# Kernel tuning notes

Measured on AMD Instinct MI355X. Metric: run time of the kernel, lower is better.

## Reference

```python
import jax, jax.numpy as jnp
import numpy as np

B, S, EMBED, DK, DV, M = 8, 1024, 1024, 512, 512, 64


def setup_inputs() -> dict:
    key = jax.random.key(0)
    ks = jax.random.split(key, 9)
    query_in = jax.random.normal(ks[0], (B, S, EMBED), dtype=jnp.float32)
    key_in = jax.random.normal(ks[1], (B, S, EMBED), dtype=jnp.float32)
    value_in = jax.random.normal(ks[2], (B, S, EMBED), dtype=jnp.float32)
    lim = 1.0 / np.sqrt(EMBED)  # nn.Linear default init range
    u = lambda k, shape: jax.random.uniform(k, shape, minval=-lim, maxval=lim, dtype=jnp.float32)
    return {
        'query_in': query_in, 'key_in': key_in, 'value_in': value_in,
        'Wq': u(ks[3], (DK, EMBED)), 'bq': u(ks[4], (DK,)),
        'Wk': u(ks[5], (DK, EMBED)), 'bk': u(ks[6], (DK,)),
        'Wv': u(ks[7], (DV, EMBED)), 'bv': u(ks[8], (DV,)),
    }


def _select_landmarks(k_proj, m):
    # Original code runs recursive RLS sampling (random, host-side) over the m
    # segment-rows of key.reshape(B, m, seg, d) and gathers m of them back,
    # then flattens to (B, S, d). We use a deterministic data-dependent
    # selection (rows ranked by squared norm) with identical gather structure.
    Bb, Ss, d = k_proj.shape
    seg = Ss // m
    kr = k_proj.reshape(Bb, m, seg, d)
    scores = jnp.sum(kr * kr, axis=(2, 3))                      # [B, m]
    idx = jnp.argsort(-scores, axis=1)                          # [B, m]
    land = jnp.take_along_axis(kr, idx[:, :, None, None], axis=1)
    return land.reshape(Bb, Ss, d)                              # [B, S, d]


def reference(query_in, key_in, value_in, Wq, bq, Wk, bk, Wv, bv):
    scaling = DK ** -0.25  # 1/sqrt(sqrt(d_k)), applied to both q and k
    q = (jnp.einsum('bse,de->bsd', query_in, Wq) + bq) * scaling
    k = (jnp.einsum('bse,de->bsd', key_in, Wk) + bk) * scaling
    v = jnp.einsum('bse,de->bsd', value_in, Wv) + bv

    kl = _select_landmarks(k, M)                                # [B, S, DK]
    # is_decoder_self_attn is hard-coded True upstream -> q_landmarks = q,
    # so kernel_2 == kernel_1.
    kernel_1 = jax.nn.softmax(jnp.einsum('bqd,bkd->bqk', q, kl), axis=-1)
    kernel_2 = kernel_1
    kernel_3 = jax.nn.softmax(jnp.einsum('bqd,bkd->bqk', q, k), axis=-1)

    k2_inv = jnp.linalg.pinv(kernel_2)                          # [B, S, S] batched SVD
    out = jnp.einsum('bqk,bkd->bqd', jnp.einsum('bqm,bmk->bqk', kernel_1, k2_inv),
                     jnp.einsum('bqk,bkd->bqd', kernel_3, v))
    # dropout is identity in eval mode
    return out
```

## Files before the change

### kernel.cpp

```cpp
#include <hip/hip_runtime.h>
#include <hip/hip_bf16.h>

#define SS   1024
#define DKK  512

typedef __hip_bfloat16 bf16;
typedef __attribute__((ext_vector_type(8))) short s16x8;
typedef __attribute__((ext_vector_type(8))) unsigned short u16x8;
typedef __attribute__((ext_vector_type(4))) float f32x4;

#define WS_W(z)  ((48ull << 20) + ((size_t)(z) << 20))
#define WS_Q     (52ull << 20)
#define WS_K     (60ull << 20)
#define WS_VT    (68ull << 20)
#define WS_LG    (0ull)

__device__ __forceinline__ void async_ld16(const void* g, void* s) {
  __builtin_amdgcn_global_load_lds(
      (const __attribute__((address_space(1))) void*)g,
      (__attribute__((address_space(3))) void*)s, 16, 0, 0);
}

__device__ __forceinline__ unsigned short f2bfu(float f) {
  return __builtin_bit_cast(unsigned short, __float2bfloat16(f));
}
__device__ __forceinline__ float bfu2f(unsigned short u) {
  unsigned int i = ((unsigned int)u) << 16;
  return __builtin_bit_cast(float, i);
}

__global__ __launch_bounds__(256)
void convert_w(const float* __restrict__ w0, const float* __restrict__ w1,
               const float* __restrict__ w2, char* __restrict__ ws)
{
  const int bx = blockIdx.x;
  const int z = bx >> 8, local = bx & 255;
  const float* src = (z == 0) ? w0 : (z == 1) ? w1 : w2;
  unsigned short* dst = (unsigned short*)(ws + WS_W(z));
  const int i = local * 2048 + threadIdx.x * 8;
  const float4* s = (const float4*)(src + i);
  float4 a = s[0], b = s[1];
  ushort4 o0, o1;
  o0.x = f2bfu(a.x); o0.y = f2bfu(a.y); o0.z = f2bfu(a.z); o0.w = f2bfu(a.w);
  o1.x = f2bfu(b.x); o1.y = f2bfu(b.y); o1.z = f2bfu(b.z); o1.w = f2bfu(b.w);
  ((ushort4*)(dst + i))[0] = o0;
  ((ushort4*)(dst + i))[1] = o1;
}

template<int BM, int K, int LDA, int LDB>
__device__ __forceinline__ void gemm_core(const bf16* __restrict__ A,
                                          const bf16* __restrict__ Bw,
                                          int bm, int bn,
                                          short* As, short* Bs, f32x4* acc)
{
  constexpr int MI = BM / 32;
  constexpr int AR = BM / 4;
  const int tid  = threadIdx.x;
  const int lane = tid & 63;
  const int wave = tid >> 6;
  const int l8   = lane >> 3;
  const int kch  = ((lane & 7) ^ l8) * 8;
  const bf16* ag = A  + (size_t)(bm * BM + wave * AR + l8) * LDA + kch;
  const bf16* bg = Bw + (size_t)(bn * 128 + wave * 32 + l8) * LDB + kch;
  short* AsW = As + wave * AR * 64;
  short* BsW = Bs + wave * 32 * 64;
  const int waveM = wave >> 1, waveN = wave & 1;
  const int l16  = lane & 15;
  const int quad = lane >> 4;
  const int xr   = l16 & 7;

  #pragma unroll
  for (int t = 0; t < MI * 4; ++t)
    #pragma unroll
    for (int r = 0; r < 4; ++r) acc[t][r] = 0.0f;

  for (int kt = 0; kt < K / 64; ++kt) {
    #pragma unroll
    for (int j = 0; j < AR / 8; ++j) async_ld16(ag + (size_t)j * 8 * LDA, AsW + j * 8 * 64);
    #pragma unroll
    for (int j = 0; j < 4; ++j)      async_ld16(bg + (size_t)j * 8 * LDB, BsW + j * 8 * 64);
    ag += 64; bg += 64;
    __syncthreads();
    #pragma unroll
    for (int ks = 0; ks < 2; ++ks) {
      s16x8 af[MI], bfv[4];
      #pragma unroll
      for (int mi = 0; mi < MI; ++mi) {
        const int row  = waveM * (BM / 2) + mi * 16 + l16;
        const int slot = (ks * 4 + quad) ^ xr;
        af[mi] = *(const s16x8*)&As[row * 64 + slot * 8];
      }
      #pragma unroll
      for (int ni = 0; ni < 4; ++ni) {
        const int row  = waveN * 64 + ni * 16 + l16;
        const int slot = (ks * 4 + quad) ^ xr;
        bfv[ni] = *(const s16x8*)&Bs[row * 64 + slot * 8];
      }
      #pragma unroll
      for (int mi = 0; mi < MI; ++mi)
        #pragma unroll
        for (int ni = 0; ni < 4; ++ni)
          acc[mi * 4 + ni] = __builtin_amdgcn_mfma_f32_16x16x32_bf16(
              af[mi], bfv[ni], acc[mi * 4 + ni], 0, 0, 0);
    }
    __syncthreads();
  }
}

template<int K, int LDA, int LDB>
__device__ __forceinline__ void gemm_core_f32a(const float* __restrict__ A,
                                               const bf16* __restrict__ Bw,
                                               int bm, int bn,
                                               short* As, short* Bs, f32x4* acc)
{
  const int tid  = threadIdx.x;
  const int lane = tid & 63;
  const int wave = tid >> 6;
  const int l8   = lane >> 3;
  const int kch  = ((lane & 7) ^ l8) * 8;
  const bf16* bg = Bw + (size_t)(bn * 256 + wave * 64 + l8) * LDB + kch;
  short* BsW = Bs + wave * 64 * 64;
  const int arow = tid >> 3;
  const int ag8  = tid & 7;
  const int slotA = (ag8 ^ (arow & 7)) * 8;
  const float* ag = A + (size_t)(bm * 64 + arow) * LDA + ag8 * 8;
  const int waveM = wave >> 1, waveN = wave & 1;
  const int l16  = lane & 15;
  const int quad = lane >> 4;
  const int xr   = l16 & 7;

  #pragma unroll
  for (int t = 0; t < 16; ++t)
    #pragma unroll
    for (int r = 0; r < 4; ++r) acc[t][r] = 0.0f;

  for (int kt = 0; kt < K / 64; ++kt) {
    #pragma unroll
    for (int j = 0; j < 8; ++j) async_ld16(bg + (size_t)j * 8 * LDB, BsW + j * 8 * 64);
    bg += 64;
    #pragma unroll
    for (int p = 0; p < 2; ++p) {
      const float4* s = (const float4*)(ag + (size_t)p * 32 * LDA);
      float4 a = s[0], b = s[1];
      u16x8 v;
      v[0] = f2bfu(a.x); v[1] = f2bfu(a.y); v[2] = f2bfu(a.z); v[3] = f2bfu(a.w);
      v[4] = f2bfu(b.x); v[5] = f2bfu(b.y); v[6] = f2bfu(b.z); v[7] = f2bfu(b.w);
      *(u16x8*)&As[(p * 32 + arow) * 64 + slotA] = v;
    }
    ag += 64;
    __syncthreads();
    #pragma unroll
    for (int ks = 0; ks < 2; ++ks) {
      s16x8 af[2], bfv[8];
      #pragma unroll
      for (int mi = 0; mi < 2; ++mi) {
        const int row  = waveM * 32 + mi * 16 + l16;
        const int slot = (ks * 4 + quad) ^ xr;
        af[mi] = *(const s16x8*)&As[row * 64 + slot * 8];
      }
      #pragma unroll
      for (int ni = 0; ni < 8; ++ni) {
        const int row  = waveN * 128 + ni * 16 + l16;
        const int slot = (ks * 4 + quad) ^ xr;
        bfv[ni] = *(const s16x8*)&Bs[row * 64 + slot * 8];
      }
      #pragma unroll
      for (int mi = 0; mi < 2; ++mi)
        #pragma unroll
        for (int ni = 0; ni < 8; ++ni)
          acc[mi * 8 + ni] = __builtin_amdgcn_mfma_f32_16x16x32_bf16(
              af[mi], bfv[ni], acc[mi * 8 + ni], 0, 0, 0);
    }
    __syncthreads();
  }
}

__global__ __launch_bounds__(256, 3)
void proj_kernel(const float* __restrict__ Xq, const float* __restrict__ Xk,
                 const float* __restrict__ Xv, const bf16* __restrict__ W0,
                 const float* __restrict__ bq, const float* __restrict__ bk,
                 const float* __restrict__ bv,
                 bf16* __restrict__ qo, bf16* __restrict__ ko,
                 bf16* __restrict__ vT, float qscale)
{
  __shared__ __align__(16) short As[64 * 64];
  __shared__ __align__(16) short Bs[256 * 64];
  const int id   = blockIdx.x;
  const int xcd  = id & 7;
  const int s    = id >> 3;
  const int bn   = s & 1;
  const int pair = (s >> 1) * 8 + xcd;
  const int bm   = pair & 127;
  const int z    = pair >> 7;
  const float* A  = (z == 0) ? Xq : (z == 1) ? Xk : Xv;
  const bf16*  Bw = W0 + ((size_t)z << 19);
  const float* bias = (z == 0) ? bq : (z == 1) ? bk : bv;
  f32x4 acc[16];
  gemm_core_f32a<1024, 1024, 1024>(A, Bw, bm, bn, As, Bs, acc);

  const int lane = threadIdx.x & 63;
  const int wave = threadIdx.x >> 6;
  const int waveM = wave >> 1, waveN = wave & 1;
  const int l16 = lane & 15, quad = lane >> 4;
  const int row0 = bm * 64 + waveM * 32;
  const int col0 = bn * 256 + waveN * 128;
  const float sc = (z == 0) ? qscale : 1.0f;
  bf16* C = (z == 0) ? qo : ko;
  #pragma unroll
  for (int ni = 0; ni < 8; ++ni) {
    const int col = col0 + ni * 16 + l16;
    const float bb = bias[col];
    #pragma unroll
    for (int mi = 0; mi < 2; ++mi)
      #pragma unroll
      for (int r = 0; r < 4; ++r) {
        const int row = row0 + mi * 16 + quad * 4 + r;
        const float v = acc[mi * 8 + ni][r] + bb;
        if (z == 2)
          vT[((size_t)(row >> 10) * DKK + col) * SS + (row & (SS - 1))] =
              __float2bfloat16(v);
        else
          C[(size_t)row * DKK + col] = __float2bfloat16(v * sc);
      }
  }
}

__global__ __launch_bounds__(256, 2)
void scores_kernel(const bf16* __restrict__ q, const bf16* __restrict__ k,
                   bf16* __restrict__ lgB)
{
  __shared__ __align__(16) short As[128 * 64];
  __shared__ __align__(16) short Bs[128 * 64];
  const int id = blockIdx.x;
  const int z  = id & 7;
  const int s  = id >> 3;
  const int bm = s & 7;
  const int bn = s >> 3;
  f32x4 acc[16];
  gemm_core<128, 512, 512, 512>(q + (size_t)z * SS * DKK, k + (size_t)z * SS * DKK,
                                bm, bn, As, Bs, acc);

  const int lane = threadIdx.x & 63;
  const int wave = threadIdx.x >> 6;
  const int waveM = wave >> 1, waveN = wave & 1;
  const int l16 = lane & 15, quad = lane >> 4;
  const int row0 = bm * 128 + waveM * 64;
  const int col0 = bn * 128 + waveN * 64;
  bf16* C = lgB + (size_t)z * SS * SS;
  #pragma unroll
  for (int ni = 0; ni < 4; ++ni) {
    const int col = col0 + ni * 16 + l16;
    #pragma unroll
    for (int mi = 0; mi < 4; ++mi)
      #pragma unroll
      for (int r = 0; r < 4; ++r) {
        const int row = row0 + mi * 16 + quad * 4 + r;
        C[(size_t)row * SS + col] = __float2bfloat16(acc[mi * 4 + ni][r]);
      }
  }
}

__global__ __launch_bounds__(256)
void softmax_p(unsigned short* __restrict__ lg)
{
  const int id = blockIdx.x;
  const int z  = id & 7;
  const int rb = id >> 3;
  const int w    = threadIdx.x >> 6;
  const int lane = threadIdx.x & 63;
  const int row  = rb * 4 + w;
  unsigned short* p = lg + ((size_t)z * SS + row) * SS + lane * 16;

  u16x8 a = *(const u16x8*)p;
  u16x8 b = *(const u16x8*)(p + 8);
  float xf[16];
  #pragma unroll
  for (int j = 0; j < 8; ++j) { xf[j] = bfu2f(a[j]); xf[8 + j] = bfu2f(b[j]); }

  float m = xf[0];
  #pragma unroll
  for (int j = 1; j < 16; ++j) m = fmaxf(m, xf[j]);
  #pragma unroll
  for (int msk = 1; msk < 64; msk <<= 1) m = fmaxf(m, __shfl_xor(m, msk));

  float e[16];
  float L = 0.f;
  #pragma unroll
  for (int j = 0; j < 16; ++j) { e[j] = __expf(xf[j] - m); L += e[j]; }
  #pragma unroll
  for (int msk = 1; msk < 64; msk <<= 1) L += __shfl_xor(L, msk);
  const float R = 1.0f / L;

  u16x8 o0, o1;
  #pragma unroll
  for (int j = 0; j < 8; ++j) {
    o0[j] = f2bfu(e[j] * R);
    o1[j] = f2bfu(e[8 + j] * R);
  }
  *(u16x8*)p = o0;
  *(u16x8*)(p + 8) = o1;
}

__global__ __launch_bounds__(256, 2)
void pv_kernel(const bf16* __restrict__ P, const bf16* __restrict__ vT,
               float* __restrict__ out)
{
  __shared__ __align__(16) short As[128 * 64];
  __shared__ __align__(16) short Bs[128 * 64];
  const int id = blockIdx.x;
  const int z  = id & 7;
  const int s  = id >> 3;
  const int bm = s & 7;
  const int bn = s >> 3;
  f32x4 acc[16];
  gemm_core<128, 1024, 1024, 1024>(P + (size_t)z * SS * SS,
                                   vT + (size_t)z * DKK * SS,
                                   bm, bn, As, Bs, acc);

  const int lane = threadIdx.x & 63;
  const int wave = threadIdx.x >> 6;
  const int waveM = wave >> 1, waveN = wave & 1;
  const int l16 = lane & 15, quad = lane >> 4;
  const int row0 = bm * 128 + waveM * 64;
  const int col0 = bn * 128 + waveN * 64;
  float* C = out + (size_t)z * SS * DKK;
  #pragma unroll
  for (int ni = 0; ni < 4; ++ni) {
    const int col = col0 + ni * 16 + l16;
    #pragma unroll
    for (int mi = 0; mi < 4; ++mi)
      #pragma unroll
      for (int r = 0; r < 4; ++r) {
        const int row = row0 + mi * 16 + quad * 4 + r;
        C[(size_t)row * DKK + col] = acc[mi * 4 + ni][r];
      }
  }
}

extern "C" void kernel_launch(void* const* d_in, const int* in_sizes, int n_in,
                              void* d_out, int out_size, void* d_ws, size_t ws_size,
                              hipStream_t stream)
{
  char* ws = (char*)d_ws;
  bf16*  W0   = (bf16*)(ws + WS_W(0));
  bf16*  q    = (bf16*)(ws + WS_Q);
  bf16*  kk   = (bf16*)(ws + WS_K);
  bf16*  vT   = (bf16*)(ws + WS_VT);
  bf16*  lgB  = (bf16*)(ws + WS_LG);

  const float qscale = 0.044194173824159216f;

  dim3 blk(256, 1, 1);
  hipLaunchKernelGGL(convert_w, dim3(768), blk, 0, stream,
                     (const float*)d_in[3], (const float*)d_in[5],
                     (const float*)d_in[7], ws);
  hipLaunchKernelGGL(proj_kernel, dim3(768, 1, 1), blk, 0, stream,
                     (const float*)d_in[0], (const float*)d_in[1],
                     (const float*)d_in[2], W0,
                     (const float*)d_in[4], (const float*)d_in[6],
                     (const float*)d_in[8], q, kk, vT, qscale);
  hipLaunchKernelGGL(scores_kernel, dim3(512, 1, 1), blk, 0, stream,
                     q, kk, lgB);
  hipLaunchKernelGGL(softmax_p, dim3(2048, 1, 1), blk, 0, stream,
                     (unsigned short*)lgB);
  hipLaunchKernelGGL(pv_kernel, dim3(256, 1, 1), blk, 0, stream,
                     lgB, vT, (float*)d_out);
}
```

Measured before the change: 217.9 us.

## Prefetch fp32 A tiles into registers and halve M tile for attention GEMMs

```diff
diff --git a/kernel.cpp b/kernel.cpp
--- a/kernel.cpp
+++ b/kernel.cpp
@@ -134,21 +134,36 @@
     #pragma unroll
     for (int r = 0; r < 4; ++r) acc[t][r] = 0.0f;
 
+  float4 a0 = ((const float4*)ag)[0];
+  float4 b0 = ((const float4*)ag)[1];
+  float4 a1 = ((const float4*)(ag + (size_t)32 * LDA))[0];
+  float4 b1 = ((const float4*)(ag + (size_t)32 * LDA))[1];
+  ag += 64;
+
   for (int kt = 0; kt < K / 64; ++kt) {
     #pragma unroll
     for (int j = 0; j < 8; ++j) async_ld16(bg + (size_t)j * 8 * LDB, BsW + j * 8 * 64);
     bg += 64;
-    #pragma unroll
-    for (int p = 0; p < 2; ++p) {
-      const float4* s = (const float4*)(ag + (size_t)p * 32 * LDA);
-      float4 a = s[0], b = s[1];
+    __builtin_amdgcn_sched_barrier(0);
+    {
       u16x8 v;
-      v[0] = f2bfu(a.x); v[1] = f2bfu(a.y); v[2] = f2bfu(a.z); v[3] = f2bfu(a.w);
-      v[4] = f2bfu(b.x); v[5] = f2bfu(b.y); v[6] = f2bfu(b.z); v[7] = f2bfu(b.w);
-      *(u16x8*)&As[(p * 32 + arow) * 64 + slotA] = v;
+      v[0] = f2bfu(a0.x); v[1] = f2bfu(a0.y); v[2] = f2bfu(a0.z); v[3] = f2bfu(a0.w);
+      v[4] = f2bfu(b0.x); v[5] = f2bfu(b0.y); v[6] = f2bfu(b0.z); v[7] = f2bfu(b0.w);
+      *(u16x8*)&As[arow * 64 + slotA] = v;
+      v[0] = f2bfu(a1.x); v[1] = f2bfu(a1.y); v[2] = f2bfu(a1.z); v[3] = f2bfu(a1.w);
+      v[4] = f2bfu(b1.x); v[5] = f2bfu(b1.y); v[6] = f2bfu(b1.z); v[7] = f2bfu(b1.w);
+      *(u16x8*)&As[(32 + arow) * 64 + slotA] = v;
     }
+    const float* agn = (kt == K / 64 - 1) ? (ag - 64) : ag;
+    float4 na0 = ((const float4*)agn)[0];
+    float4 nb0 = ((const float4*)agn)[1];
+    float4 na1 = ((const float4*)(agn + (size_t)32 * LDA))[0];
+    float4 nb1 = ((const float4*)(agn + (size_t)32 * LDA))[1];
     ag += 64;
-    __syncthreads();
+    __builtin_amdgcn_sched_barrier(0);
+    asm volatile("s_waitcnt vmcnt(4) lgkmcnt(0)" ::: "memory");
+    __builtin_amdgcn_s_barrier();
+    __builtin_amdgcn_sched_barrier(0);
     #pragma unroll
     for (int ks = 0; ks < 2; ++ks) {
       s16x8 af[2], bfv[8];
@@ -171,7 +186,11 @@
           acc[mi * 8 + ni] = __builtin_amdgcn_mfma_f32_16x16x32_bf16(
               af[mi], bfv[ni], acc[mi * 8 + ni], 0, 0, 0);
     }
-    __syncthreads();
+    __builtin_amdgcn_sched_barrier(0);
+    asm volatile("s_waitcnt lgkmcnt(0)" ::: "memory");
+    __builtin_amdgcn_s_barrier();
+    __builtin_amdgcn_sched_barrier(0);
+    a0 = na0; b0 = nb0; a1 = na1; b1 = nb1;
   }
 }
 
@@ -225,33 +244,33 @@
   }
 }
 
-__global__ __launch_bounds__(256, 2)
+__global__ __launch_bounds__(256, 4)
 void scores_kernel(const bf16* __restrict__ q, const bf16* __restrict__ k,
                    bf16* __restrict__ lgB)
 {
-  __shared__ __align__(16) short As[128 * 64];
+  __shared__ __align__(16) short As[64 * 64];
   __shared__ __align__(16) short Bs[128 * 64];
   const int id = blockIdx.x;
   const int z  = id & 7;
   const int s  = id >> 3;
-  const int bm = s & 7;
-  const int bn = s >> 3;
-  f32x4 acc[16];
-  gemm_core<128, 512, 512, 512>(q + (size_t)z * SS * DKK, k + (size_t)z * SS * DKK,
-                                bm, bn, As, Bs, acc);
+  const int bm = s & 15;
+  const int bn = s >> 4;
+  f32x4 acc[8];
+  gemm_core<64, 512, 512, 512>(q + (size_t)z * SS * DKK, k + (size_t)z * SS * DKK,
+                               bm, bn, As, Bs, acc);
 
   const int lane = threadIdx.x & 63;
   const int wave = threadIdx.x >> 6;
   const int waveM = wave >> 1, waveN = wave & 1;
   const int l16 = lane & 15, quad = lane >> 4;
-  const int row0 = bm * 128 + waveM * 64;
+  const int row0 = bm * 64 + waveM * 32;
   const int col0 = bn * 128 + waveN * 64;
   bf16* C = lgB + (size_t)z * SS * SS;
   #pragma unroll
   for (int ni = 0; ni < 4; ++ni) {
     const int col = col0 + ni * 16 + l16;
     #pragma unroll
-    for (int mi = 0; mi < 4; ++mi)
+    for (int mi = 0; mi < 2; ++mi)
       #pragma unroll
       for (int r = 0; r < 4; ++r) {
         const int row = row0 + mi * 16 + quad * 4 + r;
@@ -301,34 +320,34 @@
   *(u16x8*)(p + 8) = o1;
 }
 
-__global__ __launch_bounds__(256, 2)
+__global__ __launch_bounds__(256, 4)
 void pv_kernel(const bf16* __restrict__ P, const bf16* __restrict__ vT,
                float* __restrict__ out)
 {
-  __shared__ __align__(16) short As[128 * 64];
+  __shared__ __align__(16) short As[64 * 64];
   __shared__ __align__(16) short Bs[128 * 64];
   const int id = blockIdx.x;
   const int z  = id & 7;
   const int s  = id >> 3;
-  const int bm = s & 7;
-  const int bn = s >> 3;
-  f32x4 acc[16];
-  gemm_core<128, 1024, 1024, 1024>(P + (size_t)z * SS * SS,
-                                   vT + (size_t)z * DKK * SS,
-                                   bm, bn, As, Bs, acc);
+  const int bm = s & 15;
+  const int bn = s >> 4;
+  f32x4 acc[8];
+  gemm_core<64, 1024, 1024, 1024>(P + (size_t)z * SS * SS,
+                                  vT + (size_t)z * DKK * SS,
+                                  bm, bn, As, Bs, acc);
 
   const int lane = threadIdx.x & 63;
   const int wave = threadIdx.x >> 6;
   const int waveM = wave >> 1, waveN = wave & 1;
   const int l16 = lane & 15, quad = lane >> 4;
-  const int row0 = bm * 128 + waveM * 64;
+  const int row0 = bm * 64 + waveM * 32;
   const int col0 = bn * 128 + waveN * 64;
   float* C = out + (size_t)z * SS * DKK;
   #pragma unroll
   for (int ni = 0; ni < 4; ++ni) {
     const int col = col0 + ni * 16 + l16;
     #pragma unroll
-    for (int mi = 0; mi < 4; ++mi)
+    for (int mi = 0; mi < 2; ++mi)
       #pragma unroll
       for (int r = 0; r < 4; ++r) {
         const int row = row0 + mi * 16 + quad * 4 + r;
@@ -359,10 +378,10 @@
                      (const float*)d_in[2], W0,
                      (const float*)d_in[4], (const float*)d_in[6],
                      (const float*)d_in[8], q, kk, vT, qscale);
-  hipLaunchKernelGGL(scores_kernel, dim3(512, 1, 1), blk, 0, stream,
+  hipLaunchKernelGGL(scores_kernel, dim3(1024, 1, 1), blk, 0, stream,
                      q, kk, lgB);
   hipLaunchKernelGGL(softmax_p, dim3(2048, 1, 1), blk, 0, stream,
                      (unsigned short*)lgB);
-  hipLaunchKernelGGL(pv_kernel, dim3(256, 1, 1), blk, 0, stream,
+  hipLaunchKernelGGL(pv_kernel, dim3(512, 1, 1), blk, 0, stream,
                      lgB, vT, (float*)d_out);
 }
```

Result: faster. 210.1 us (-3.6%).
